# Kernel tuning notes

Hardware: AMD Instinct MI355X
Metric: run time of the kernel (lower is better)

Reference implementation:

```python
import jax, jax.numpy as jnp
import numpy as np
from jax import lax

KD, KH, KW = 9, 9, 9  # box-filter window (matches torch ones([1,1,9,9,9]))


def _box_sum(x):
    """Sum over a 9x9x9 window with SAME (zero) padding, via separable 1D convs.
    x: [B, 1, D, H, W]. Mathematically identical to conv3d with an all-ones
    9x9x9 kernel, but O(3k) instead of O(k^3) work per voxel.
    """
    dn = ('NCDHW', 'OIDHW', 'NCDHW')
    dt = x.dtype
    kd = jnp.ones((1, 1, KD, 1, 1), dt)
    kh = jnp.ones((1, 1, 1, KH, 1), dt)
    kw = jnp.ones((1, 1, 1, 1, KW), dt)
    pd, ph, pw = (KD - 1) // 2, (KH - 1) // 2, (KW - 1) // 2
    x = lax.conv_general_dilated(x, kd, (1, 1, 1), [(pd, pd), (0, 0), (0, 0)], dimension_numbers=dn)
    x = lax.conv_general_dilated(x, kh, (1, 1, 1), [(0, 0), (ph, ph), (0, 0)], dimension_numbers=dn)
    x = lax.conv_general_dilated(x, kw, (1, 1, 1), [(0, 0), (0, 0), (pw, pw)], dimension_numbers=dn)
    return x


def setup_inputs() -> dict:
    key = jax.random.key(0)
    k1, k2 = jax.random.split(key)
    shape = (2, 1, 160, 192, 160)  # [B, C=1, D, H, W]
    return {
        'input': jax.random.normal(k1, shape, dtype=jnp.float32),
        'target': jax.random.normal(k2, shape, dtype=jnp.float32),
    }


def reference(input, target):
    ksize = jnp.asarray(KD * KH * KW, input.dtype)
    I_sum = _box_sum(input)
    T_sum = _box_sum(target)
    II_sum = _box_sum(input * input)
    TT_sum = _box_sum(target * target)
    IT_sum = _box_sum(input * target)

    Ihat = I_sum / ksize
    That = T_sum / ksize
    cross = IT_sum - Ihat * T_sum - That * I_sum + That * Ihat * ksize
    T_var = TT_sum - 2 * That * T_sum + That * That * ksize
    I_var = II_sum - 2 * Ihat * I_sum + Ihat * Ihat * ksize
    cc = cross * cross / (T_var * I_var + 1e-5)
    return -1.0 * jnp.mean(cc)
```

## Files before the change

kernel.cpp:

```cpp
#include <hip/hip_runtime.h>

#define DIM_W 160
#define DIM_H 192
#define DIM_D 160
#define DIM_B 2

constexpr int TW = 16;
constexpr int TH = 32;
constexpr int CH = 19;
constexpr int NCH = 9;
constexpr int RH = TH + 8;
constexpr float INV_K = 1.0f / 729.0f;
constexpr double NTOT = 9830400.0;

typedef unsigned int u32;
typedef __attribute__((address_space(1))) const u32 gu32;
typedef __attribute__((address_space(3))) u32 lu32;

__global__ void init_kernel(float* out, float* ws) {
    out[0] = 0.0f;
    ws[0] = 0.0f; ws[1] = 0.0f; ws[2] = 0.0f; ws[3] = 0.0f;
}

__device__ __forceinline__ int clampD(int s) {
    return s < 0 ? 0 : (s > DIM_D - 1 ? DIM_D - 1 : s);
}

__global__ __launch_bounds__(256)
void lncc3d_kernel(const float* __restrict__ I,
                   const float* __restrict__ T,
                   const float* __restrict__ zsrc,
                   float* __restrict__ out)
{
    __shared__ __align__(16) float sR[2][2][RH][32];
    __shared__ __align__(16) float4 wA[RH][16];
    __shared__ __align__(16) float  wB[16][44];
    __shared__ float red[4];

    const int tid  = threadIdx.x;
    const int lane = tid & 63;
    const int wid  = tid >> 6;
    const int wo   = tid & 15;
    const int hb   = (tid >> 4) << 1;

    const int bw = blockIdx.x, bh = blockIdx.y, bz = blockIdx.z;
    const int b  = bz / NCH;
    const int c  = bz - b * NCH;
    const int w0 = bw * TW, h0 = bh * TH, d0 = c * CH;
    const int dEnd = min(d0 + CH, DIM_D);

    const int plane = DIM_H * DIM_W;
    const int fld  = wid >> 1;
    const int kodd = wid & 1;
    const int nck  = kodd ? 2 : 3;
    const float* Fb = (fld ? T : I) + (size_t)b * DIM_D * plane;

    int boff[3], crw[3];
#pragma unroll
    for (int i = 0; i < 3; ++i) {
        const int ck  = kodd ? (2 * i + 1) : (2 * i);
        const int row = 8 * ck + (lane >> 3);
        const int pf4 = lane & 7;
        const int lf4 = (pf4 - row) & 7;
        const int gh  = h0 - 4 + row;
        const int gw  = w0 - 8 + (lf4 << 2);
        crw[i]  = 8 * ck;
        boff[i] = (i < nck && gh >= 0 && gh < DIM_H && gw >= 0 && gw <= DIM_W - 4)
                  ? (gh * DIM_W + gw) : -1;
    }

    auto issue = [&](int sc, int buf) {
        const float* Fs = Fb + (size_t)sc * plane;
#pragma unroll
        for (int i = 0; i < 3; ++i) {
            if (i < nck) {
                const float* gp = (boff[i] >= 0) ? (Fs + boff[i]) : zsrc;
                __builtin_amdgcn_global_load_lds((gu32*)gp, (lu32*)&sR[buf][fld][crw[i]][0],
                                                 16, 0, 0);
            }
        }
    };

    float rgI[2][9], rgT[2][9], rgII[2][9], rgTT[2][9], rgIT[2][9];
    float rnI[2], rnT[2], rnII[2], rnTT[2], rnIT[2];
#pragma unroll
    for (int p = 0; p < 2; ++p) {
        rnI[p] = rnT[p] = rnII[p] = rnTT[p] = rnIT[p] = 0.0f;
#pragma unroll
        for (int q = 0; q < 9; ++q) {
            rgI[p][q] = rgT[p][q] = rgII[p][q] = rgTT[p][q] = rgIT[p][q] = 0.0f;
        }
    }
    float acc = 0.0f;

    const int sStart = d0 - 4;
    int cur = 0;

    issue(clampD(sStart), 0);
    issue(clampD(sStart + 1), 1);
    if (kodd) { asm volatile("s_waitcnt vmcnt(2)" ::: "memory"); }
    else      { asm volatile("s_waitcnt vmcnt(3)" ::: "memory"); }
    __builtin_amdgcn_s_barrier();

    for (int t = 0; t < 3; ++t) {
        const int t9 = t * 9;
#pragma unroll
        for (int j = 0; j < 9; ++j) {
            const int s  = sStart + t9 + j;
            const bool vs = (s >= 0) && (s < DIM_D);

            if (vs && tid < 160) {
                const int r = tid >> 2;
                const int g = tid & 3;
                const float* rIp = &sR[cur][0][r][0];
                const float* rTp = &sR[cur][1][r][0];
                const int q0 = ((g + 1 + r) & 7) << 2;
                const int q1 = ((g + 2 + r) & 7) << 2;
                const int q2 = ((g + 3 + r) & 7) << 2;
                const float4 ia  = *(const float4*)(rIp + q0);
                const float4 ib4 = *(const float4*)(rIp + q1);
                const float4 ic4 = *(const float4*)(rIp + q2);
                const float4 ta  = *(const float4*)(rTp + q0);
                const float4 tb4 = *(const float4*)(rTp + q1);
                const float4 tc4 = *(const float4*)(rTp + q2);
                const float iv[12] = {ia.x, ia.y, ia.z, ia.w, ib4.x, ib4.y, ib4.z, ib4.w,
                                      ic4.x, ic4.y, ic4.z, ic4.w};
                const float tv[12] = {ta.x, ta.y, ta.z, ta.w, tb4.x, tb4.y, tb4.z, tb4.w,
                                      tc4.x, tc4.y, tc4.z, tc4.w};
                float aI = 0.f, aT = 0.f, aII = 0.f, aTT = 0.f, aIT = 0.f;
#pragma unroll
                for (int k = 0; k < 9; ++k) {
                    aI += iv[k]; aT += tv[k];
                    aII = fmaf(iv[k], iv[k], aII);
                    aTT = fmaf(tv[k], tv[k], aTT);
                    aIT = fmaf(iv[k], tv[k], aIT);
                }
                const int c0 = g << 2;
                wA[r][(c0 + r) & 15] = make_float4(aI, aT, aII, aTT);
                wB[c0][r] = aIT;
#pragma unroll
                for (int q = 1; q < 4; ++q) {
                    const float ni = iv[8 + q], oi = iv[q - 1];
                    const float nt = tv[8 + q], ot = tv[q - 1];
                    aI += ni - oi; aT += nt - ot;
                    aII = fmaf(ni, ni, fmaf(oi, -oi, aII));
                    aTT = fmaf(nt, nt, fmaf(ot, -ot, aTT));
                    aIT = fmaf(ni, nt, fmaf(oi, -ot, aIT));
                    wA[r][(c0 + q + r) & 15] = make_float4(aI, aT, aII, aTT);
                    wB[c0 + q][r] = aIT;
                }
            }
            asm volatile("s_waitcnt lgkmcnt(0)" ::: "memory");
            __builtin_amdgcn_s_barrier();

            issue(clampD(s + 2), cur);

            float s2I0, s2T0, s2II0, s2TT0, s2IT0, s2I1, s2T1, s2II1, s2TT1, s2IT1;
            if (vs) {
                const float4 A0 = wA[hb][(wo + hb) & 15];
                float sx = A0.x, sy = A0.y, szv = A0.z, swv = A0.w;
#pragma unroll
                for (int k = 1; k < 9; ++k) {
                    const float4 Ak = wA[hb + k][(wo + hb + k) & 15];
                    sx += Ak.x; sy += Ak.y; szv += Ak.z; swv += Ak.w;
                }
                const float4 A9 = wA[hb + 9][(wo + hb + 9) & 15];
                const float2 B0 = *(const float2*)&wB[wo][hb];
                const float2 B1 = *(const float2*)&wB[wo][hb + 2];
                const float2 B2 = *(const float2*)&wB[wo][hb + 4];
                const float2 B3 = *(const float2*)&wB[wo][hb + 6];
                const float2 B4 = *(const float2*)&wB[wo][hb + 8];
                const float sbv = B0.x + B0.y + B1.x + B1.y + B2.x + B2.y
                                + B3.x + B3.y + B4.x;
                s2I0 = sx; s2T0 = sy; s2II0 = szv; s2TT0 = swv; s2IT0 = sbv;
                s2I1  = sx  - A0.x + A9.x;
                s2T1  = sy  - A0.y + A9.y;
                s2II1 = szv - A0.z + A9.z;
                s2TT1 = swv - A0.w + A9.w;
                s2IT1 = sbv - B0.x + B4.y;
            } else {
                s2I0 = s2T0 = s2II0 = s2TT0 = s2IT0 = 0.f;
                s2I1 = s2T1 = s2II1 = s2TT1 = s2IT1 = 0.f;
            }

            rnI[0]  += s2I0  - rgI[0][j];  rgI[0][j]  = s2I0;
            rnT[0]  += s2T0  - rgT[0][j];  rgT[0][j]  = s2T0;
            rnII[0] += s2II0 - rgII[0][j]; rgII[0][j] = s2II0;
            rnTT[0] += s2TT0 - rgTT[0][j]; rgTT[0][j] = s2TT0;
            rnIT[0] += s2IT0 - rgIT[0][j]; rgIT[0][j] = s2IT0;
            rnI[1]  += s2I1  - rgI[1][j];  rgI[1][j]  = s2I1;
            rnT[1]  += s2T1  - rgT[1][j];  rgT[1][j]  = s2T1;
            rnII[1] += s2II1 - rgII[1][j]; rgII[1][j] = s2II1;
            rnTT[1] += s2TT1 - rgTT[1][j]; rgTT[1][j] = s2TT1;
            rnIT[1] += s2IT1 - rgIT[1][j]; rgIT[1][j] = s2IT1;

            if ((s >= d0 + 4) && ((s - 4) < dEnd)) {
                float cr, vv, tvv;
                cr  = rnIT[0] - rnI[0] * rnT[0] * INV_K;
                vv  = rnII[0] - rnI[0] * rnI[0] * INV_K;
                tvv = rnTT[0] - rnT[0] * rnT[0] * INV_K;
                acc += cr * cr * __builtin_amdgcn_rcpf(fmaf(tvv, vv, 1e-5f));
                cr  = rnIT[1] - rnI[1] * rnT[1] * INV_K;
                vv  = rnII[1] - rnI[1] * rnI[1] * INV_K;
                tvv = rnTT[1] - rnT[1] * rnT[1] * INV_K;
                acc += cr * cr * __builtin_amdgcn_rcpf(fmaf(tvv, vv, 1e-5f));
            }

            asm volatile("s_waitcnt lgkmcnt(0)" ::: "memory");
            if (kodd) { asm volatile("s_waitcnt vmcnt(2)" ::: "memory"); }
            else      { asm volatile("s_waitcnt vmcnt(3)" ::: "memory"); }
            __builtin_amdgcn_s_barrier();
            cur ^= 1;
        }
    }

#pragma unroll
    for (int off = 32; off > 0; off >>= 1) acc += __shfl_down(acc, off, 64);
    if (lane == 0) red[wid] = acc;
    __syncthreads();
    if (tid == 0) {
        const float bs = red[0] + red[1] + red[2] + red[3];
        atomicAdd(out, bs * (float)(-1.0 / NTOT));
    }
}

extern "C" void kernel_launch(void* const* d_in, const int* in_sizes, int n_in,
                              void* d_out, int out_size, void* d_ws, size_t ws_size,
                              hipStream_t stream) {
    const float* I = (const float*)d_in[0];
    const float* T = (const float*)d_in[1];
    float* out = (float*)d_out;
    float* ws  = (float*)d_ws;

    init_kernel<<<dim3(1), dim3(1), 0, stream>>>(out, ws);

    dim3 grid(DIM_W / TW, DIM_H / TH, DIM_B * NCH);
    dim3 block(256);
    lncc3d_kernel<<<grid, block, 0, stream>>>(I, T, ws, out);
}
```

Measured before the change: 83.04 us.

## Enlarge H tile to 48 rows with three outputs per thread

Raises the H tile height from 32 to 48, so each thread now produces three H-adjacent output columns instead of two, sliding the H-direction window sum across them. The load distribution across waves, the LDS buffers, the thread count for the W pass and the vmcnt waits are all reworked to match. The aim is to cut the halo overhead (8 extra rows per tile) and spread the per-plane barrier and sync cost over more output, at the price of more registers (extra running sums and ring buffers) and fewer blocks in the grid.

Measured after the change: 103.7 us. 1.25x slower.

```diff
diff --git a/kernel.cpp b/kernel.cpp
--- a/kernel.cpp
+++ b/kernel.cpp
@@ -6,7 +6,7 @@
 #define DIM_B 2
 
 constexpr int TW = 16;
-constexpr int TH = 32;
+constexpr int TH = 48;
 constexpr int CH = 19;
 constexpr int NCH = 9;
 constexpr int RH = TH + 8;
@@ -34,14 +34,14 @@
 {
     __shared__ __align__(16) float sR[2][2][RH][32];
     __shared__ __align__(16) float4 wA[RH][16];
-    __shared__ __align__(16) float  wB[16][44];
+    __shared__ __align__(16) float  wB[16][60];
     __shared__ float red[4];
 
     const int tid  = threadIdx.x;
     const int lane = tid & 63;
     const int wid  = tid >> 6;
     const int wo   = tid & 15;
-    const int hb   = (tid >> 4) << 1;
+    const int hb   = (tid >> 4) * 3;
 
     const int bw = blockIdx.x, bh = blockIdx.y, bz = blockIdx.z;
     const int b  = bz / NCH;
@@ -51,14 +51,14 @@
 
     const int plane = DIM_H * DIM_W;
     const int fld  = wid >> 1;
-    const int kodd = wid & 1;
-    const int nck  = kodd ? 2 : 3;
+    const int khi  = wid & 1;
+    const int nck  = khi ? 3 : 4;
     const float* Fb = (fld ? T : I) + (size_t)b * DIM_D * plane;
 
-    int boff[3], crw[3];
-#pragma unroll
-    for (int i = 0; i < 3; ++i) {
-        const int ck  = kodd ? (2 * i + 1) : (2 * i);
+    int boff[4], crw[4];
+#pragma unroll
+    for (int i = 0; i < 4; ++i) {
+        const int ck  = khi ? (4 + i) : i;
         const int row = 8 * ck + (lane >> 3);
         const int pf4 = lane & 7;
         const int lf4 = (pf4 - row) & 7;
@@ -72,7 +72,7 @@
     auto issue = [&](int sc, int buf) {
         const float* Fs = Fb + (size_t)sc * plane;
 #pragma unroll
-        for (int i = 0; i < 3; ++i) {
+        for (int i = 0; i < 4; ++i) {
             if (i < nck) {
                 const float* gp = (boff[i] >= 0) ? (Fs + boff[i]) : zsrc;
                 __builtin_amdgcn_global_load_lds((gu32*)gp, (lu32*)&sR[buf][fld][crw[i]][0],
@@ -81,10 +81,10 @@
         }
     };
 
-    float rgI[2][9], rgT[2][9], rgII[2][9], rgTT[2][9], rgIT[2][9];
-    float rnI[2], rnT[2], rnII[2], rnTT[2], rnIT[2];
-#pragma unroll
-    for (int p = 0; p < 2; ++p) {
+    float rgI[3][9], rgT[3][9], rgII[3][9], rgTT[3][9], rgIT[3][9];
+    float rnI[3], rnT[3], rnII[3], rnTT[3], rnIT[3];
+#pragma unroll
+    for (int p = 0; p < 3; ++p) {
         rnI[p] = rnT[p] = rnII[p] = rnTT[p] = rnIT[p] = 0.0f;
 #pragma unroll
         for (int q = 0; q < 9; ++q) {
@@ -98,8 +98,8 @@
 
     issue(clampD(sStart), 0);
     issue(clampD(sStart + 1), 1);
-    if (kodd) { asm volatile("s_waitcnt vmcnt(2)" ::: "memory"); }
-    else      { asm volatile("s_waitcnt vmcnt(3)" ::: "memory"); }
+    if (khi) { asm volatile("s_waitcnt vmcnt(3)" ::: "memory"); }
+    else     { asm volatile("s_waitcnt vmcnt(4)" ::: "memory"); }
     __builtin_amdgcn_s_barrier();
 
     for (int t = 0; t < 3; ++t) {
@@ -109,7 +109,7 @@
             const int s  = sStart + t9 + j;
             const bool vs = (s >= 0) && (s < DIM_D);
 
-            if (vs && tid < 160) {
+            if (vs && tid < 224) {
                 const int r = tid >> 2;
                 const int g = tid & 3;
                 const float* rIp = &sR[cur][0][r][0];
@@ -155,60 +155,73 @@
 
             issue(clampD(s + 2), cur);
 
-            float s2I0, s2T0, s2II0, s2TT0, s2IT0, s2I1, s2T1, s2II1, s2TT1, s2IT1;
+            float s2I[3], s2T[3], s2II[3], s2TT[3], s2IT[3];
             if (vs) {
-                const float4 A0 = wA[hb][(wo + hb) & 15];
-                float sx = A0.x, sy = A0.y, szv = A0.z, swv = A0.w;
-#pragma unroll
-                for (int k = 1; k < 9; ++k) {
-                    const float4 Ak = wA[hb + k][(wo + hb + k) & 15];
-                    sx += Ak.x; sy += Ak.y; szv += Ak.z; swv += Ak.w;
-                }
-                const float4 A9 = wA[hb + 9][(wo + hb + 9) & 15];
-                const float2 B0 = *(const float2*)&wB[wo][hb];
-                const float2 B1 = *(const float2*)&wB[wo][hb + 2];
-                const float2 B2 = *(const float2*)&wB[wo][hb + 4];
-                const float2 B3 = *(const float2*)&wB[wo][hb + 6];
-                const float2 B4 = *(const float2*)&wB[wo][hb + 8];
-                const float sbv = B0.x + B0.y + B1.x + B1.y + B2.x + B2.y
-                                + B3.x + B3.y + B4.x;
-                s2I0 = sx; s2T0 = sy; s2II0 = szv; s2TT0 = swv; s2IT0 = sbv;
-                s2I1  = sx  - A0.x + A9.x;
-                s2T1  = sy  - A0.y + A9.y;
-                s2II1 = szv - A0.z + A9.z;
-                s2TT1 = swv - A0.w + A9.w;
-                s2IT1 = sbv - B0.x + B4.y;
+#define RDA(k) wA[hb + (k)][(wo + hb + (k)) & 15]
+                const float4 A0 = RDA(0);
+                const float4 A1 = RDA(1);
+                float sx = A0.x + A1.x, sy = A0.y + A1.y;
+                float sz = A0.z + A1.z, sw = A0.w + A1.w;
+#pragma unroll
+                for (int k = 2; k < 9; ++k) {
+                    const float4 Ak = RDA(k);
+                    sx += Ak.x; sy += Ak.y; sz += Ak.z; sw += Ak.w;
+                }
+                s2I[0] = sx; s2T[0] = sy; s2II[0] = sz; s2TT[0] = sw;
+                const float4 A9 = RDA(9);
+                const float p1x = sx - A0.x + A9.x, p1y = sy - A0.y + A9.y;
+                const float p1z = sz - A0.z + A9.z, p1w = sw - A0.w + A9.w;
+                s2I[1] = p1x; s2T[1] = p1y; s2II[1] = p1z; s2TT[1] = p1w;
+                const float4 A10 = RDA(10);
+                s2I[2]  = p1x - A1.x + A10.x;
+                s2T[2]  = p1y - A1.y + A10.y;
+                s2II[2] = p1z - A1.z + A10.z;
+                s2TT[2] = p1w - A1.w + A10.w;
+#undef RDA
+                const int  base = hb & ~1;
+                const bool od   = (hb & 1) != 0;
+                const float* wp = &wB[wo][base];
+                const float2 e0 = *(const float2*)(wp);
+                const float2 e1 = *(const float2*)(wp + 2);
+                const float2 e2 = *(const float2*)(wp + 4);
+                const float2 e3 = *(const float2*)(wp + 6);
+                const float2 e4 = *(const float2*)(wp + 8);
+                const float2 e5 = *(const float2*)(wp + 10);
+                const float2 e6 = *(const float2*)(wp + 12);
+                const float f0 = e0.x, f1 = e0.y, f2 = e1.x, f3 = e1.y;
+                const float f4 = e2.x, f5 = e2.y, f6 = e3.x, f7 = e3.y;
+                const float f8 = e4.x, f9 = e4.y, f10 = e5.x, f11 = e5.y;
+                const float pre9 = f0 + f1 + f2 + f3 + f4 + f5 + f6 + f7 + f8;
+                const float it0 = od ? (pre9 - f0 + f9) : pre9;
+                const float it1 = it0 - (od ? f1 : f0) + (od ? f10 : f9);
+                const float it2 = it1 - (od ? f2 : f1) + (od ? f11 : f10);
+                s2IT[0] = it0; s2IT[1] = it1; s2IT[2] = it2;
             } else {
-                s2I0 = s2T0 = s2II0 = s2TT0 = s2IT0 = 0.f;
-                s2I1 = s2T1 = s2II1 = s2TT1 = s2IT1 = 0.f;
-            }
-
-            rnI[0]  += s2I0  - rgI[0][j];  rgI[0][j]  = s2I0;
-            rnT[0]  += s2T0  - rgT[0][j];  rgT[0][j]  = s2T0;
-            rnII[0] += s2II0 - rgII[0][j]; rgII[0][j] = s2II0;
-            rnTT[0] += s2TT0 - rgTT[0][j]; rgTT[0][j] = s2TT0;
-            rnIT[0] += s2IT0 - rgIT[0][j]; rgIT[0][j] = s2IT0;
-            rnI[1]  += s2I1  - rgI[1][j];  rgI[1][j]  = s2I1;
-            rnT[1]  += s2T1  - rgT[1][j];  rgT[1][j]  = s2T1;
-            rnII[1] += s2II1 - rgII[1][j]; rgII[1][j] = s2II1;
-            rnTT[1] += s2TT1 - rgTT[1][j]; rgTT[1][j] = s2TT1;
-            rnIT[1] += s2IT1 - rgIT[1][j]; rgIT[1][j] = s2IT1;
-
-            if ((s >= d0 + 4) && ((s - 4) < dEnd)) {
-                float cr, vv, tvv;
-                cr  = rnIT[0] - rnI[0] * rnT[0] * INV_K;
-                vv  = rnII[0] - rnI[0] * rnI[0] * INV_K;
-                tvv = rnTT[0] - rnT[0] * rnT[0] * INV_K;
-                acc += cr * cr * __builtin_amdgcn_rcpf(fmaf(tvv, vv, 1e-5f));
-                cr  = rnIT[1] - rnI[1] * rnT[1] * INV_K;
-                vv  = rnII[1] - rnI[1] * rnI[1] * INV_K;
-                tvv = rnTT[1] - rnT[1] * rnT[1] * INV_K;
-                acc += cr * cr * __builtin_amdgcn_rcpf(fmaf(tvv, vv, 1e-5f));
+#pragma unroll
+                for (int p = 0; p < 3; ++p) {
+                    s2I[p] = s2T[p] = s2II[p] = s2TT[p] = s2IT[p] = 0.f;
+                }
+            }
+
+            const bool em = (s >= d0 + 4) && ((s - 4) < dEnd);
+#pragma unroll
+            for (int p = 0; p < 3; ++p) {
+                rnI[p]  += s2I[p]  - rgI[p][j];  rgI[p][j]  = s2I[p];
+                rnT[p]  += s2T[p]  - rgT[p][j];  rgT[p][j]  = s2T[p];
+                rnII[p] += s2II[p] - rgII[p][j]; rgII[p][j] = s2II[p];
+                rnTT[p] += s2TT[p] - rgTT[p][j]; rgTT[p][j] = s2TT[p];
+                rnIT[p] += s2IT[p] - rgIT[p][j]; rgIT[p][j] = s2IT[p];
+                if (em) {
+                    const float cr  = rnIT[p] - rnI[p] * rnT[p] * INV_K;
+                    const float vv  = rnII[p] - rnI[p] * rnI[p] * INV_K;
+                    const float tvv = rnTT[p] - rnT[p] * rnT[p] * INV_K;
+                    acc += cr * cr * __builtin_amdgcn_rcpf(fmaf(tvv, vv, 1e-5f));
+                }
             }
 
             asm volatile("s_waitcnt lgkmcnt(0)" ::: "memory");
-            if (kodd) { asm volatile("s_waitcnt vmcnt(2)" ::: "memory"); }
-            else      { asm volatile("s_waitcnt vmcnt(3)" ::: "memory"); }
+            if (khi) { asm volatile("s_waitcnt vmcnt(3)" ::: "memory"); }
+            else     { asm volatile("s_waitcnt vmcnt(4)" ::: "memory"); }
             __builtin_amdgcn_s_barrier();
             cur ^= 1;
         }
```

## Precompute H-pair sums via DPP and compact the W-halo slab layout

Applied to the files above, without the earlier changes.

Each thread that computes W-direction window sums now also builds pairwise sums of adjacent rows using DPP lane shifts. These pair sums go into new shared arrays, so the H-direction 9-row sum reads four pair sums plus one row instead of nine rows. The input slab load now uses a dense 24-float row stride with a 4-column halo instead of the 32-wide swizzled layout, which cuts the global-to-LDS loads from three chunks per wave to two. The cost is more shared memory and extra DPP and LDS stores in the first phase, and correctness depends on the DPP direction detection and on the paired rows sitting in adjacent lanes.

Result: slower. 90.76 us (+9.3%).

```diff
diff --git a/kernel.cpp b/kernel.cpp
--- a/kernel.cpp
+++ b/kernel.cpp
@@ -10,6 +10,7 @@
 constexpr int CH = 19;
 constexpr int NCH = 9;
 constexpr int RH = TH + 8;
+constexpr int RWDS = 24;
 constexpr float INV_K = 1.0f / 729.0f;
 constexpr double NTOT = 9830400.0;
 
@@ -24,6 +25,15 @@
 
 __device__ __forceinline__ int clampD(int s) {
     return s < 0 ? 0 : (s > DIM_D - 1 ? DIM_D - 1 : s);
+}
+
+__device__ __forceinline__ float pairsum(float v, bool dirA) {
+    const int vi = __builtin_bit_cast(int, v);
+    const int aa = __builtin_amdgcn_update_dpp(0, vi, 0x104, 0xF, 0xF, true);
+    const int bb = __builtin_amdgcn_update_dpp(0, vi, 0x114, 0xF, 0xF, true);
+    const float fa = __builtin_bit_cast(float, aa);
+    const float fb = __builtin_bit_cast(float, bb);
+    return v + (dirA ? fa : fb);
 }
 
 __global__ __launch_bounds__(256)
@@ -32,16 +42,19 @@
                    const float* __restrict__ zsrc,
                    float* __restrict__ out)
 {
-    __shared__ __align__(16) float sR[2][2][RH][32];
+    __shared__ __align__(16) float sR[2][2][1024];
     __shared__ __align__(16) float4 wA[RH][16];
     __shared__ __align__(16) float  wB[16][44];
+    __shared__ __align__(16) float4 g2A[20][17];
+    __shared__ float  g2B[16][22];
     __shared__ float red[4];
 
     const int tid  = threadIdx.x;
     const int lane = tid & 63;
     const int wid  = tid >> 6;
     const int wo   = tid & 15;
-    const int hb   = (tid >> 4) << 1;
+    const int p0   = tid >> 4;
+    const int hb   = p0 << 1;
 
     const int bw = blockIdx.x, bh = blockIdx.y, bz = blockIdx.z;
     const int b  = bz / NCH;
@@ -50,34 +63,34 @@
     const int dEnd = min(d0 + CH, DIM_D);
 
     const int plane = DIM_H * DIM_W;
-    const int fld  = wid >> 1;
-    const int kodd = wid & 1;
-    const int nck  = kodd ? 2 : 3;
+    const int fld = wid >> 1;
+    const int khi = wid & 1;
     const float* Fb = (fld ? T : I) + (size_t)b * DIM_D * plane;
 
-    int boff[3], crw[3];
-#pragma unroll
-    for (int i = 0; i < 3; ++i) {
-        const int ck  = kodd ? (2 * i + 1) : (2 * i);
-        const int row = 8 * ck + (lane >> 3);
-        const int pf4 = lane & 7;
-        const int lf4 = (pf4 - row) & 7;
+    const int shp = __builtin_amdgcn_update_dpp(0, lane, 0x104, 0xF, 0xF, true);
+    const bool dirA = (__builtin_amdgcn_readfirstlane(shp) == 4);
+
+    int boff[2], ldof[2];
+#pragma unroll
+    for (int i = 0; i < 2; ++i) {
+        const int ck  = (khi << 1) | i;
+        const int s16 = ck * 64 + lane;
+        const int row = s16 / 6;
+        const int q   = s16 - row * 6;
         const int gh  = h0 - 4 + row;
-        const int gw  = w0 - 8 + (lf4 << 2);
-        crw[i]  = 8 * ck;
-        boff[i] = (i < nck && gh >= 0 && gh < DIM_H && gw >= 0 && gw <= DIM_W - 4)
+        const int gw  = w0 - 4 + (q << 2);
+        ldof[i] = ck << 8;
+        boff[i] = (row < RH && gh >= 0 && gh < DIM_H && gw >= 0 && gw <= DIM_W - 4)
                   ? (gh * DIM_W + gw) : -1;
     }
 
     auto issue = [&](int sc, int buf) {
         const float* Fs = Fb + (size_t)sc * plane;
 #pragma unroll
-        for (int i = 0; i < 3; ++i) {
-            if (i < nck) {
-                const float* gp = (boff[i] >= 0) ? (Fs + boff[i]) : zsrc;
-                __builtin_amdgcn_global_load_lds((gu32*)gp, (lu32*)&sR[buf][fld][crw[i]][0],
-                                                 16, 0, 0);
-            }
+        for (int i = 0; i < 2; ++i) {
+            const float* gp = (boff[i] >= 0) ? (Fs + boff[i]) : zsrc;
+            __builtin_amdgcn_global_load_lds((gu32*)gp, (lu32*)&sR[buf][fld][ldof[i]],
+                                             16, 0, 0);
         }
     };
 
@@ -98,8 +111,7 @@
 
     issue(clampD(sStart), 0);
     issue(clampD(sStart + 1), 1);
-    if (kodd) { asm volatile("s_waitcnt vmcnt(2)" ::: "memory"); }
-    else      { asm volatile("s_waitcnt vmcnt(3)" ::: "memory"); }
+    asm volatile("s_waitcnt vmcnt(2)" ::: "memory");
     __builtin_amdgcn_s_barrier();
 
     for (int t = 0; t < 3; ++t) {
@@ -110,44 +122,58 @@
             const bool vs = (s >= 0) && (s < DIM_D);
 
             if (vs && tid < 160) {
-                const int r = tid >> 2;
-                const int g = tid & 3;
-                const float* rIp = &sR[cur][0][r][0];
-                const float* rTp = &sR[cur][1][r][0];
-                const int q0 = ((g + 1 + r) & 7) << 2;
-                const int q1 = ((g + 2 + r) & 7) << 2;
-                const int q2 = ((g + 3 + r) & 7) << 2;
-                const float4 ia  = *(const float4*)(rIp + q0);
-                const float4 ib4 = *(const float4*)(rIp + q1);
-                const float4 ic4 = *(const float4*)(rIp + q2);
-                const float4 ta  = *(const float4*)(rTp + q0);
-                const float4 tb4 = *(const float4*)(rTp + q1);
-                const float4 tc4 = *(const float4*)(rTp + q2);
+                const int r  = tid >> 2;
+                const int g  = tid & 3;
+                const int c0 = g << 2;
+                const float* rIp = &sR[cur][0][r * RWDS];
+                const float* rTp = &sR[cur][1][r * RWDS];
+                const float4 ia  = *(const float4*)(rIp + c0);
+                const float4 ib4 = *(const float4*)(rIp + c0 + 4);
+                const float4 ic4 = *(const float4*)(rIp + c0 + 8);
+                const float4 ta  = *(const float4*)(rTp + c0);
+                const float4 tb4 = *(const float4*)(rTp + c0 + 4);
+                const float4 tc4 = *(const float4*)(rTp + c0 + 8);
                 const float iv[12] = {ia.x, ia.y, ia.z, ia.w, ib4.x, ib4.y, ib4.z, ib4.w,
                                       ic4.x, ic4.y, ic4.z, ic4.w};
                 const float tv[12] = {ta.x, ta.y, ta.z, ta.w, tb4.x, tb4.y, tb4.z, tb4.w,
                                       tc4.x, tc4.y, tc4.z, tc4.w};
-                float aI = 0.f, aT = 0.f, aII = 0.f, aTT = 0.f, aIT = 0.f;
-#pragma unroll
-                for (int k = 0; k < 9; ++k) {
-                    aI += iv[k]; aT += tv[k];
-                    aII = fmaf(iv[k], iv[k], aII);
-                    aTT = fmaf(tv[k], tv[k], aTT);
-                    aIT = fmaf(iv[k], tv[k], aIT);
+                float vI[4], vT[4], vII[4], vTT[4], vIT[4];
+                {
+                    float aI = 0.f, aT = 0.f, aII = 0.f, aTT = 0.f, aIT = 0.f;
+#pragma unroll
+                    for (int k = 0; k < 9; ++k) {
+                        aI += iv[k]; aT += tv[k];
+                        aII = fmaf(iv[k], iv[k], aII);
+                        aTT = fmaf(tv[k], tv[k], aTT);
+                        aIT = fmaf(iv[k], tv[k], aIT);
+                    }
+                    vI[0] = aI; vT[0] = aT; vII[0] = aII; vTT[0] = aTT; vIT[0] = aIT;
+#pragma unroll
+                    for (int q = 1; q < 4; ++q) {
+                        const float ni = iv[8 + q], oi = iv[q - 1];
+                        const float nt = tv[8 + q], ot = tv[q - 1];
+                        aI += ni - oi; aT += nt - ot;
+                        aII = fmaf(ni, ni, fmaf(oi, -oi, aII));
+                        aTT = fmaf(nt, nt, fmaf(ot, -ot, aTT));
+                        aIT = fmaf(ni, nt, fmaf(oi, -ot, aIT));
+                        vI[q] = aI; vT[q] = aT; vII[q] = aII; vTT[q] = aTT; vIT[q] = aIT;
+                    }
                 }
-                const int c0 = g << 2;
-                wA[r][(c0 + r) & 15] = make_float4(aI, aT, aII, aTT);
-                wB[c0][r] = aIT;
-#pragma unroll
-                for (int q = 1; q < 4; ++q) {
-                    const float ni = iv[8 + q], oi = iv[q - 1];
-                    const float nt = tv[8 + q], ot = tv[q - 1];
-                    aI += ni - oi; aT += nt - ot;
-                    aII = fmaf(ni, ni, fmaf(oi, -oi, aII));
-                    aTT = fmaf(nt, nt, fmaf(ot, -ot, aTT));
-                    aIT = fmaf(ni, nt, fmaf(oi, -ot, aIT));
-                    wA[r][(c0 + q + r) & 15] = make_float4(aI, aT, aII, aTT);
-                    wB[c0 + q][r] = aIT;
+                const bool ev = ((r & 1) == 0);
+                const int  r2 = r >> 1;
+#pragma unroll
+                for (int q = 0; q < 4; ++q) {
+                    wA[r][(c0 + q + r) & 15] = make_float4(vI[q], vT[q], vII[q], vTT[q]);
+                    wB[c0 + q][r] = vIT[q];
+                    const float gI  = pairsum(vI[q],  dirA);
+                    const float gT  = pairsum(vT[q],  dirA);
+                    const float gII = pairsum(vII[q], dirA);
+                    const float gTT = pairsum(vTT[q], dirA);
+                    const float gIT = pairsum(vIT[q], dirA);
+                    if (ev) {
+                        g2A[r2][c0 + q] = make_float4(gI, gT, gII, gTT);
+                        g2B[c0 + q][r2] = gIT;
+                    }
                 }
             }
             asm volatile("s_waitcnt lgkmcnt(0)" ::: "memory");
@@ -157,27 +183,25 @@
 
             float s2I0, s2T0, s2II0, s2TT0, s2IT0, s2I1, s2T1, s2II1, s2TT1, s2IT1;
             if (vs) {
-                const float4 A0 = wA[hb][(wo + hb) & 15];
-                float sx = A0.x, sy = A0.y, szv = A0.z, swv = A0.w;
-#pragma unroll
-                for (int k = 1; k < 9; ++k) {
-                    const float4 Ak = wA[hb + k][(wo + hb + k) & 15];
-                    sx += Ak.x; sy += Ak.y; szv += Ak.z; swv += Ak.w;
-                }
-                const float4 A9 = wA[hb + 9][(wo + hb + 9) & 15];
-                const float2 B0 = *(const float2*)&wB[wo][hb];
-                const float2 B1 = *(const float2*)&wB[wo][hb + 2];
-                const float2 B2 = *(const float2*)&wB[wo][hb + 4];
-                const float2 B3 = *(const float2*)&wB[wo][hb + 6];
-                const float2 B4 = *(const float2*)&wB[wo][hb + 8];
-                const float sbv = B0.x + B0.y + B1.x + B1.y + B2.x + B2.y
-                                + B3.x + B3.y + B4.x;
-                s2I0 = sx; s2T0 = sy; s2II0 = szv; s2TT0 = swv; s2IT0 = sbv;
-                s2I1  = sx  - A0.x + A9.x;
-                s2T1  = sy  - A0.y + A9.y;
-                s2II1 = szv - A0.z + A9.z;
-                s2TT1 = swv - A0.w + A9.w;
-                s2IT1 = sbv - B0.x + B4.y;
+                const float4 G0 = g2A[p0][wo];
+                const float4 G1 = g2A[p0 + 1][wo];
+                const float4 G2_ = g2A[p0 + 2][wo];
+                const float4 G3 = g2A[p0 + 3][wo];
+                const float4 R8 = wA[hb + 8][(wo + hb + 8) & 15];
+                const float4 R0 = wA[hb][(wo + hb) & 15];
+                const float4 R9 = wA[hb + 9][(wo + hb + 9) & 15];
+                s2I0  = G0.x + G1.x + G2_.x + G3.x + R8.x;
+                s2T0  = G0.y + G1.y + G2_.y + G3.y + R8.y;
+                s2II0 = G0.z + G1.z + G2_.z + G3.z + R8.z;
+                s2TT0 = G0.w + G1.w + G2_.w + G3.w + R8.w;
+                s2I1  = s2I0  - R0.x + R9.x;
+                s2T1  = s2T0  - R0.y + R9.y;
+                s2II1 = s2II0 - R0.z + R9.z;
+                s2TT1 = s2TT0 - R0.w + R9.w;
+                const float itg = g2B[wo][p0] + g2B[wo][p0 + 1]
+                                + g2B[wo][p0 + 2] + g2B[wo][p0 + 3];
+                s2IT0 = itg + wB[wo][hb + 8];
+                s2IT1 = s2IT0 - wB[wo][hb] + wB[wo][hb + 9];
             } else {
                 s2I0 = s2T0 = s2II0 = s2TT0 = s2IT0 = 0.f;
                 s2I1 = s2T1 = s2II1 = s2TT1 = s2IT1 = 0.f;
@@ -207,8 +231,7 @@
             }
 
             asm volatile("s_waitcnt lgkmcnt(0)" ::: "memory");
-            if (kodd) { asm volatile("s_waitcnt vmcnt(2)" ::: "memory"); }
-            else      { asm volatile("s_waitcnt vmcnt(3)" ::: "memory"); }
+            asm volatile("s_waitcnt vmcnt(2)" ::: "memory");
             __builtin_amdgcn_s_barrier();
             cur ^= 1;
         }
```
